# Kernel tuning notes

Measured on AMD Instinct MI355X. Metric: run time of the kernel, lower is better.

Reference implementation:

```python
import jax, jax.numpy as jnp
import numpy as np

H, D_IN, D_Q, D_V = 8, 16, 32, 32
N = M = 4096


def setup_inputs() -> dict:
    key = jax.random.key(0)
    ks = jax.random.split(key, 12)
    s_in = 1.0 / np.sqrt(D_IN)
    s_fc = 1.0 / np.sqrt(H * D_V)
    return {
        "x": jax.random.normal(ks[0], (N, D_IN), jnp.float32),
        "y": jax.random.normal(ks[1], (M, D_IN), jnp.float32),
        # per-head stacked weights: [H, D_IN, D_Q/ D_V]
        "Wq": jax.random.uniform(ks[2], (H, D_IN, D_Q), jnp.float32, -s_in, s_in),
        "bq": jax.random.uniform(ks[3], (H, D_Q), jnp.float32, -s_in, s_in),
        "Wk": jax.random.uniform(ks[4], (H, D_IN, D_Q), jnp.float32, -s_in, s_in),
        "bk": jax.random.uniform(ks[5], (H, D_Q), jnp.float32, -s_in, s_in),
        "Wv": jax.random.uniform(ks[6], (H, D_IN, D_V), jnp.float32, -s_in, s_in),
        "bv": jax.random.uniform(ks[7], (H, D_V), jnp.float32, -s_in, s_in),
        "Wo": jax.random.uniform(ks[8], (H * D_V, D_IN), jnp.float32, -s_fc, s_fc),
        "bo": jax.random.uniform(ks[9], (D_IN,), jnp.float32, -s_fc, s_fc),
    }


def reference(x, y, Wq, bq, Wk, bk, Wv, bv, Wo, bo):
    # batched per-head projections (fuses the 8 tiny Linears of the torch loop)
    q = jnp.einsum("nd,hdq->hnq", x, Wq) + bq[:, None, :]   # [H, N, D_Q]
    k = jnp.einsum("md,hdq->hmq", y, Wk) + bk[:, None, :]   # [H, M, D_Q]
    v = jnp.einsum("md,hdv->hmv", y, Wv) + bv[:, None, :]   # [H, M, D_V]
    scores = jnp.einsum("hnq,hmq->hnm", q, k) / jnp.sqrt(jnp.float32(D_Q))
    attn = jax.nn.softmax(scores, axis=-1)                  # [H, N, M]
    heads = jnp.einsum("hnm,hmv->hnv", attn, v)             # [H, N, D_V]
    # torch.cat(head_outputs, dim=-1): head h occupies columns [h*D_V:(h+1)*D_V]
    concat = jnp.transpose(heads, (1, 0, 2)).reshape(x.shape[0], H * D_V)
    return concat @ Wo + bo                                  # [N, D_IN]
```

## Files before the change

kernel.cpp:

```cpp
#include <hip/hip_runtime.h>
#include <hip/hip_bf16.h>

typedef __attribute__((ext_vector_type(8))) short bf16x8;
typedef __attribute__((ext_vector_type(4))) float f32x4;
typedef unsigned short u16;
typedef unsigned int u32;

#define NH 8
#define NN 4096
#define MM 4096

__device__ __forceinline__ u16 f2bf(float f) {
  u32 b = __float_as_uint(f);
  b += 0x7FFFu + ((b >> 16) & 1u);
  return (u16)(b >> 16);
}

__device__ __forceinline__ u32 pack_rnu(float a, float b) {
  u32 ua = __float_as_uint(a) + 0x8000u;
  u32 ub = __float_as_uint(b) + 0x8000u;
#if __has_builtin(__builtin_amdgcn_perm)
  return __builtin_amdgcn_perm(ub, ua, 0x07060302u);
#else
  return (ua >> 16) | (ub & 0xFFFF0000u);
#endif
}

#if __has_builtin(__builtin_amdgcn_exp2f)
__device__ __forceinline__ float exp2_fast(float x) { return __builtin_amdgcn_exp2f(x); }
#else
__device__ __forceinline__ float exp2_fast(float x) { return __expf(x * 0.69314718055994531f); }
#endif

__global__ __launch_bounds__(256) void proj_kernel(
    const float* __restrict__ x, const float* __restrict__ y,
    const float* __restrict__ Wq, const float* __restrict__ bq,
    const float* __restrict__ Wk, const float* __restrict__ bk,
    const float* __restrict__ Wv, const float* __restrict__ bv,
    u16* __restrict__ qs, u16* __restrict__ ks, u16* __restrict__ vT)
{
  __shared__ u16 sv[256][33];
  const int bid = blockIdx.x;
  const int tid = threadIdx.x;
  if (bid < 256) {
    int idx = bid * 256 + tid;
    int t = idx >> 15;
    int h = (idx >> 12) & 7;
    int row = idx & 4095;
    const float* src = (t ? y : x) + row * 16;
    const float* W = (t ? Wk : Wq) + (h << 9);
    const float* b = (t ? bk : bq) + (h << 5);
    const float scale = t ? 1.0f : 0.25503635116465163f;
    float4 r4[4];
#pragma unroll
    for (int i = 0; i < 4; ++i) r4[i] = ((const float4*)src)[i];
    const float* r = (const float*)r4;
    u16* out = (t ? ks : qs) + (idx & 32767) * 32;
#pragma unroll
    for (int j = 0; j < 32; ++j) {
      float a = b[j];
#pragma unroll
      for (int i = 0; i < 16; ++i) a = fmaf(r[i], W[i * 32 + j], a);
      out[j] = f2bf(a * scale);
    }
  } else {
    int vb = bid - 256;
    int h = vb >> 4;
    int kb = (vb & 15) << 8;
    const float* src = y + (kb + tid) * 16;
    const float* W = Wv + (h << 9);
    const float* b = bv + (h << 5);
    float4 r4[4];
#pragma unroll
    for (int i = 0; i < 4; ++i) r4[i] = ((const float4*)src)[i];
    const float* r = (const float*)r4;
#pragma unroll
    for (int j = 0; j < 32; ++j) {
      float a = b[j];
#pragma unroll
      for (int i = 0; i < 16; ++i) a = fmaf(r[i], W[i * 32 + j], a);
      sv[tid][j] = f2bf(a);
    }
    __syncthreads();
    int dv = tid >> 3;
    int c = (tid & 7) << 5;
    u16* dst = vT + (((h << 5) + dv) << 12) + kb + c;
#pragma unroll
    for (int q = 0; q < 4; ++q) {
      uint4 w;
      w.x = (u32)sv[c + 4 * q + 0][dv]      | ((u32)sv[c + 4 * q + 1][dv] << 16);
      w.y = (u32)sv[c + 4 * q + 2][dv]      | ((u32)sv[c + 4 * q + 3][dv] << 16);
      w.z = (u32)sv[c + 16 + 4 * q + 0][dv] | ((u32)sv[c + 16 + 4 * q + 1][dv] << 16);
      w.w = (u32)sv[c + 16 + 4 * q + 2][dv] | ((u32)sv[c + 16 + 4 * q + 3][dv] << 16);
      *(uint4*)(dst + q * 8) = w;
    }
  }
}

#define KST 40
#define VST 72
#define VSZ (32 * VST)

__global__ __launch_bounds__(256) void flash_kernel(
    const u16* __restrict__ qs, const u16* __restrict__ ksrc,
    const u16* __restrict__ vT, float* __restrict__ accP,
    float* __restrict__ lsumP)
{
  __shared__ u16 sK[128 * KST];
  __shared__ u16 sVT[2 * VSZ];
  const int h = blockIdx.y;
  const int qt = blockIdx.x;
  const int z = blockIdx.z;
  const int nIter = (MM / 128) / gridDim.z;
  const int kb0 = z * (MM / gridDim.z);
  const int tid = threadIdx.x;
  const int wv = tid >> 6;
  const int lane = tid & 63;
  const int d = lane & 15;
  const int g = lane >> 4;
  const int qrowA = (qt << 7) + (wv << 5) + d;
  const int qrowB = qrowA + 16;

  union U4 { uint4 q; bf16x8 v; };
  U4 qfA, qfB;
  qfA.q = *(const uint4*)(qs + (((h << 12) + qrowA) << 5) + (g << 3));
  qfB.q = *(const uint4*)(qs + (((h << 12) + qrowB) << 5) + (g << 3));

  union { u32 w[4]; bf16x8 v; } ones;
  {
    u32 ow = (d == 0) ? 0x3F803F80u : 0u;
    ones.w[0] = ow; ones.w[1] = ow; ones.w[2] = ow; ones.w[3] = ow;
  }

  f32x4 accA0 = {0.f, 0.f, 0.f, 0.f}, accA1 = {0.f, 0.f, 0.f, 0.f};
  f32x4 accB0 = {0.f, 0.f, 0.f, 0.f}, accB1 = {0.f, 0.f, 0.f, 0.f};
  f32x4 accLA = {0.f, 0.f, 0.f, 0.f}, accLB = {0.f, 0.f, 0.f, 0.f};
  const f32x4 zero = {0.f, 0.f, 0.f, 0.f};

  const u16* gK = ksrc + (h << 17) + (kb0 << 5) + ((tid >> 1) << 5) + ((tid & 1) << 4);
  const u16* gV = vT + (((h << 5) + (tid >> 3)) << 12) + kb0 + ((tid & 7) << 4);
  u16* wK = sK + (tid >> 1) * KST + ((tid & 1) << 4);
  u16* wV = sVT + ((tid & 7) >> 2) * VSZ + (tid >> 3) * VST + ((tid & 7) & 3) * 16;

  {
    uint4 a = *(const uint4*)gK, b = *(const uint4*)(gK + 8);
    uint4 c = *(const uint4*)gV, e = *(const uint4*)(gV + 8);
    *(uint4*)wK = a; *(uint4*)(wK + 8) = b;
    *(uint4*)wV = c; *(uint4*)(wV + 8) = e;
  }
  __syncthreads();

  auto compute = [&](const u16* kb, const u16* vb) {
    U4 kf[4];
#pragma unroll
    for (int t = 0; t < 4; ++t)
      kf[t].q = *(const uint4*)(kb + (t * 16 + d) * KST + (g << 3));

    union { u32 w[4]; bf16x8 v; } pbA0, pbA1, pbB0, pbB1;
    {
      f32x4 s0, s1, s2, s3;
      s0 = __builtin_amdgcn_mfma_f32_16x16x32_bf16(kf[0].v, qfA.v, zero, 0, 0, 0);
      s1 = __builtin_amdgcn_mfma_f32_16x16x32_bf16(kf[1].v, qfA.v, zero, 0, 0, 0);
      s2 = __builtin_amdgcn_mfma_f32_16x16x32_bf16(kf[2].v, qfA.v, zero, 0, 0, 0);
      s3 = __builtin_amdgcn_mfma_f32_16x16x32_bf16(kf[3].v, qfA.v, zero, 0, 0, 0);
      float e[16];
      e[0]=exp2_fast(s0.x); e[1]=exp2_fast(s0.y); e[2]=exp2_fast(s0.z); e[3]=exp2_fast(s0.w);
      e[4]=exp2_fast(s1.x); e[5]=exp2_fast(s1.y); e[6]=exp2_fast(s1.z); e[7]=exp2_fast(s1.w);
      e[8]=exp2_fast(s2.x); e[9]=exp2_fast(s2.y); e[10]=exp2_fast(s2.z); e[11]=exp2_fast(s2.w);
      e[12]=exp2_fast(s3.x); e[13]=exp2_fast(s3.y); e[14]=exp2_fast(s3.z); e[15]=exp2_fast(s3.w);
      pbA0.w[0] = pack_rnu(e[0], e[1]);   pbA0.w[1] = pack_rnu(e[2], e[3]);
      pbA0.w[2] = pack_rnu(e[4], e[5]);   pbA0.w[3] = pack_rnu(e[6], e[7]);
      pbA1.w[0] = pack_rnu(e[8], e[9]);   pbA1.w[1] = pack_rnu(e[10], e[11]);
      pbA1.w[2] = pack_rnu(e[12], e[13]); pbA1.w[3] = pack_rnu(e[14], e[15]);
    }
    {
      f32x4 s0, s1, s2, s3;
      s0 = __builtin_amdgcn_mfma_f32_16x16x32_bf16(kf[0].v, qfB.v, zero, 0, 0, 0);
      s1 = __builtin_amdgcn_mfma_f32_16x16x32_bf16(kf[1].v, qfB.v, zero, 0, 0, 0);
      s2 = __builtin_amdgcn_mfma_f32_16x16x32_bf16(kf[2].v, qfB.v, zero, 0, 0, 0);
      s3 = __builtin_amdgcn_mfma_f32_16x16x32_bf16(kf[3].v, qfB.v, zero, 0, 0, 0);
      float e[16];
      e[0]=exp2_fast(s0.x); e[1]=exp2_fast(s0.y); e[2]=exp2_fast(s0.z); e[3]=exp2_fast(s0.w);
      e[4]=exp2_fast(s1.x); e[5]=exp2_fast(s1.y); e[6]=exp2_fast(s1.z); e[7]=exp2_fast(s1.w);
      e[8]=exp2_fast(s2.x); e[9]=exp2_fast(s2.y); e[10]=exp2_fast(s2.z); e[11]=exp2_fast(s2.w);
      e[12]=exp2_fast(s3.x); e[13]=exp2_fast(s3.y); e[14]=exp2_fast(s3.z); e[15]=exp2_fast(s3.w);
      pbB0.w[0] = pack_rnu(e[0], e[1]);   pbB0.w[1] = pack_rnu(e[2], e[3]);
      pbB0.w[2] = pack_rnu(e[4], e[5]);   pbB0.w[3] = pack_rnu(e[6], e[7]);
      pbB1.w[0] = pack_rnu(e[8], e[9]);   pbB1.w[1] = pack_rnu(e[10], e[11]);
      pbB1.w[2] = pack_rnu(e[12], e[13]); pbB1.w[3] = pack_rnu(e[14], e[15]);
    }
    accLA = __builtin_amdgcn_mfma_f32_16x16x32_bf16(ones.v, pbA0.v, accLA, 0, 0, 0);
    accLA = __builtin_amdgcn_mfma_f32_16x16x32_bf16(ones.v, pbA1.v, accLA, 0, 0, 0);
    accLB = __builtin_amdgcn_mfma_f32_16x16x32_bf16(ones.v, pbB0.v, accLB, 0, 0, 0);
    accLB = __builtin_amdgcn_mfma_f32_16x16x32_bf16(ones.v, pbB1.v, accLB, 0, 0, 0);
    U4 vf0, vf1, vf2, vf3;
    const u16* vp = vb + d * VST;
    vf0.q = *(const uint4*)(vp + (g << 3));
    vf1.q = *(const uint4*)(vp + 32 + (g << 3));
    vp += 16 * VST;
    vf2.q = *(const uint4*)(vp + (g << 3));
    vf3.q = *(const uint4*)(vp + 32 + (g << 3));
    accA0 = __builtin_amdgcn_mfma_f32_16x16x32_bf16(vf0.v, pbA0.v, accA0, 0, 0, 0);
    accA0 = __builtin_amdgcn_mfma_f32_16x16x32_bf16(vf1.v, pbA1.v, accA0, 0, 0, 0);
    accA1 = __builtin_amdgcn_mfma_f32_16x16x32_bf16(vf2.v, pbA0.v, accA1, 0, 0, 0);
    accA1 = __builtin_amdgcn_mfma_f32_16x16x32_bf16(vf3.v, pbA1.v, accA1, 0, 0, 0);
    accB0 = __builtin_amdgcn_mfma_f32_16x16x32_bf16(vf0.v, pbB0.v, accB0, 0, 0, 0);
    accB0 = __builtin_amdgcn_mfma_f32_16x16x32_bf16(vf1.v, pbB1.v, accB0, 0, 0, 0);
    accB1 = __builtin_amdgcn_mfma_f32_16x16x32_bf16(vf2.v, pbB0.v, accB1, 0, 0, 0);
    accB1 = __builtin_amdgcn_mfma_f32_16x16x32_bf16(vf3.v, pbB1.v, accB1, 0, 0, 0);
  };

#pragma unroll 1
  for (int it = 0; it < nIter; ++it) {
    uint4 a, b, c, e;
    if (it < nIter - 1) {
      gK += 4096; gV += 128;
      a = *(const uint4*)gK; b = *(const uint4*)(gK + 8);
      c = *(const uint4*)gV; e = *(const uint4*)(gV + 8);
    }
    compute(sK, sVT);
    compute(sK + 64 * KST, sVT + VSZ);
    __syncthreads();
    if (it < nIter - 1) {
      *(uint4*)wK = a; *(uint4*)(wK + 8) = b;
      *(uint4*)wV = c; *(uint4*)(wV + 8) = e;
      __syncthreads();
    }
  }

  if (g == 0) {
    lsumP[((z * NH + h) << 12) + qrowA] = accLA.x;
    lsumP[((z * NH + h) << 12) + qrowB] = accLB.x;
  }
  float* cpA = accP + z * (NN * 256) + (qrowA << 8) + (h << 5) + (g << 2);
  *(float4*)cpA        = make_float4(accA0.x, accA0.y, accA0.z, accA0.w);
  *(float4*)(cpA + 16) = make_float4(accA1.x, accA1.y, accA1.z, accA1.w);
  float* cpB = accP + z * (NN * 256) + (qrowB << 8) + (h << 5) + (g << 2);
  *(float4*)cpB        = make_float4(accB0.x, accB0.y, accB0.z, accB0.w);
  *(float4*)(cpB + 16) = make_float4(accB1.x, accB1.y, accB1.z, accB1.w);
}

__global__ __launch_bounds__(256) void out_fused_kernel(
    const float* __restrict__ accP, const float* __restrict__ lsumP,
    const float* __restrict__ Wo, const float* __restrict__ bo,
    float* __restrict__ out, int S)
{
  __shared__ float cn[4][256];
  __shared__ float sQ[4][4][16];
  const int tid = threadIdx.x;
  const int n0 = blockIdx.x << 2;

  {
    const int r = tid >> 6, u = tid & 63;
    const int n = n0 + r;
    float4 o = make_float4(0.f, 0.f, 0.f, 0.f);
    for (int s = 0; s < S; ++s) {
      const float4 v = *(const float4*)(accP + (size_t)s * (NN * 256) + (n << 8) + (u << 2));
      o.x += v.x; o.y += v.y; o.z += v.z; o.w += v.w;
    }
    const int hh = u >> 3;
    float l = 0.f;
    for (int s = 0; s < S; ++s) l += lsumP[((s * NH + hh) << 12) + n];
    const float inv = 1.0f / l;
    *(float4*)&cn[r][u << 2] = make_float4(o.x * inv, o.y * inv, o.z * inv, o.w * inv);
  }
  __syncthreads();

  {
    const int r = tid >> 6, ks = (tid >> 4) & 3, c = tid & 15;
    const float* cr = &cn[r][ks << 6];
    const float* wp = Wo + (ks << 6) * 16 + c;
    float a = 0.f;
#pragma unroll
    for (int jj = 0; jj < 64; ++jj) {
      const int j2 = (jj + (ks << 4)) & 63;
      a = fmaf(cr[j2], wp[j2 * 16], a);
    }
    sQ[r][ks][c] = a;
  }
  __syncthreads();

  if (tid < 64) {
    const int r = tid >> 4, c = tid & 15;
    float v = bo[c] + ((sQ[r][0][c] + sQ[r][1][c]) + (sQ[r][2][c] + sQ[r][3][c]));
    out[((n0 + r) << 4) + c] = v;
  }
}

extern "C" void kernel_launch(void* const* d_in, const int* in_sizes, int n_in,
                              void* d_out, int out_size, void* d_ws, size_t ws_size,
                              hipStream_t stream) {
  const float* x  = (const float*)d_in[0];
  const float* y  = (const float*)d_in[1];
  const float* Wq = (const float*)d_in[2];
  const float* bq = (const float*)d_in[3];
  const float* Wk = (const float*)d_in[4];
  const float* bk = (const float*)d_in[5];
  const float* Wv = (const float*)d_in[6];
  const float* bv = (const float*)d_in[7];
  const float* Wo = (const float*)d_in[8];
  const float* bo = (const float*)d_in[9];
  float* out = (float*)d_out;

  u16* qs = (u16*)d_ws;
  u16* ks = qs + (NH * NN * 32);
  u16* vT = ks + (NH * MM * 32);
  float* accP = (float*)(vT + (NH * MM * 32));
  const int S = (ws_size >= (size_t)(6 + 16) * 1024 * 1024 + 512 * 1024) ? 4 : 1;
  float* lsumP = accP + (size_t)S * (NN * 256);

  hipLaunchKernelGGL(proj_kernel, dim3(384), dim3(256), 0, stream,
                     x, y, Wq, bq, Wk, bk, Wv, bv, qs, ks, vT);
  hipLaunchKernelGGL(flash_kernel, dim3(32, NH, S), dim3(256), 0, stream,
                     qs, ks, vT, accP, lsumP);
  hipLaunchKernelGGL(out_fused_kernel, dim3(1024), dim3(256), 0, stream,
                     accP, lsumP, Wo, bo, out, S);
}
```

Before: 62.45 us.

## Double query rows per warp and compute row sums with VALU adds

Each wave now handles 64 query rows instead of 32, so every K/V fragment read from LDS is reused across four query tiles, and the grid's query dimension is halved. The softmax denominator is now accumulated with scalar float adds and cross-lane shuffles instead of extra MFMAs against a ones vector. This cuts LDS traffic and MFMA count per score. The cost is more registers and fewer blocks (16x8xS), which may lower occupancy and parallelism on a 256-CU device.

New measurement: 64.97 us. 1.04x slower.

```diff
diff --git a/kernel.cpp b/kernel.cpp
--- a/kernel.cpp
+++ b/kernel.cpp
@@ -118,23 +118,26 @@
   const int lane = tid & 63;
   const int d = lane & 15;
   const int g = lane >> 4;
-  const int qrowA = (qt << 7) + (wv << 5) + d;
+  const int qrowA = (qt << 8) + (wv << 6) + d;
   const int qrowB = qrowA + 16;
+  const int qrowC = qrowA + 32;
+  const int qrowD = qrowA + 48;
 
   union U4 { uint4 q; bf16x8 v; };
-  U4 qfA, qfB;
-  qfA.q = *(const uint4*)(qs + (((h << 12) + qrowA) << 5) + (g << 3));
-  qfB.q = *(const uint4*)(qs + (((h << 12) + qrowB) << 5) + (g << 3));
-
-  union { u32 w[4]; bf16x8 v; } ones;
+  U4 qfA, qfB, qfC, qfD;
   {
-    u32 ow = (d == 0) ? 0x3F803F80u : 0u;
-    ones.w[0] = ow; ones.w[1] = ow; ones.w[2] = ow; ones.w[3] = ow;
-  }
-
+    const u16* qb = qs + (((h << 12) + qrowA) << 5) + (g << 3);
+    qfA.q = *(const uint4*)qb;
+    qfB.q = *(const uint4*)(qb + (16 << 5));
+    qfC.q = *(const uint4*)(qb + (32 << 5));
+    qfD.q = *(const uint4*)(qb + (48 << 5));
+  }
+
+  float lsA = 0.f, lsB = 0.f, lsC = 0.f, lsD = 0.f;
   f32x4 accA0 = {0.f, 0.f, 0.f, 0.f}, accA1 = {0.f, 0.f, 0.f, 0.f};
   f32x4 accB0 = {0.f, 0.f, 0.f, 0.f}, accB1 = {0.f, 0.f, 0.f, 0.f};
-  f32x4 accLA = {0.f, 0.f, 0.f, 0.f}, accLB = {0.f, 0.f, 0.f, 0.f};
+  f32x4 accC0 = {0.f, 0.f, 0.f, 0.f}, accC1 = {0.f, 0.f, 0.f, 0.f};
+  f32x4 accD0 = {0.f, 0.f, 0.f, 0.f}, accD1 = {0.f, 0.f, 0.f, 0.f};
   const f32x4 zero = {0.f, 0.f, 0.f, 0.f};
 
   const u16* gK = ksrc + (h << 17) + (kb0 << 5) + ((tid >> 1) << 5) + ((tid & 1) << 4);
@@ -151,63 +154,52 @@
   __syncthreads();
 
   auto compute = [&](const u16* kb, const u16* vb) {
-    U4 kf[4];
-#pragma unroll
-    for (int t = 0; t < 4; ++t)
-      kf[t].q = *(const uint4*)(kb + (t * 16 + d) * KST + (g << 3));
-
-    union { u32 w[4]; bf16x8 v; } pbA0, pbA1, pbB0, pbB1;
+    U4 kf0, kf1, kf2, kf3;
+    kf0.q = *(const uint4*)(kb + (0 * 16 + d) * KST + (g << 3));
+    kf1.q = *(const uint4*)(kb + (1 * 16 + d) * KST + (g << 3));
+    kf2.q = *(const uint4*)(kb + (2 * 16 + d) * KST + (g << 3));
+    kf3.q = *(const uint4*)(kb + (3 * 16 + d) * KST + (g << 3));
+    U4 vf0, vf1, vf2, vf3;
     {
-      f32x4 s0, s1, s2, s3;
-      s0 = __builtin_amdgcn_mfma_f32_16x16x32_bf16(kf[0].v, qfA.v, zero, 0, 0, 0);
-      s1 = __builtin_amdgcn_mfma_f32_16x16x32_bf16(kf[1].v, qfA.v, zero, 0, 0, 0);
-      s2 = __builtin_amdgcn_mfma_f32_16x16x32_bf16(kf[2].v, qfA.v, zero, 0, 0, 0);
-      s3 = __builtin_amdgcn_mfma_f32_16x16x32_bf16(kf[3].v, qfA.v, zero, 0, 0, 0);
-      float e[16];
-      e[0]=exp2_fast(s0.x); e[1]=exp2_fast(s0.y); e[2]=exp2_fast(s0.z); e[3]=exp2_fast(s0.w);
-      e[4]=exp2_fast(s1.x); e[5]=exp2_fast(s1.y); e[6]=exp2_fast(s1.z); e[7]=exp2_fast(s1.w);
-      e[8]=exp2_fast(s2.x); e[9]=exp2_fast(s2.y); e[10]=exp2_fast(s2.z); e[11]=exp2_fast(s2.w);
-      e[12]=exp2_fast(s3.x); e[13]=exp2_fast(s3.y); e[14]=exp2_fast(s3.z); e[15]=exp2_fast(s3.w);
-      pbA0.w[0] = pack_rnu(e[0], e[1]);   pbA0.w[1] = pack_rnu(e[2], e[3]);
-      pbA0.w[2] = pack_rnu(e[4], e[5]);   pbA0.w[3] = pack_rnu(e[6], e[7]);
-      pbA1.w[0] = pack_rnu(e[8], e[9]);   pbA1.w[1] = pack_rnu(e[10], e[11]);
-      pbA1.w[2] = pack_rnu(e[12], e[13]); pbA1.w[3] = pack_rnu(e[14], e[15]);
-    }
-    {
-      f32x4 s0, s1, s2, s3;
-      s0 = __builtin_amdgcn_mfma_f32_16x16x32_bf16(kf[0].v, qfB.v, zero, 0, 0, 0);
-      s1 = __builtin_amdgcn_mfma_f32_16x16x32_bf16(kf[1].v, qfB.v, zero, 0, 0, 0);
-      s2 = __builtin_amdgcn_mfma_f32_16x16x32_bf16(kf[2].v, qfB.v, zero, 0, 0, 0);
-      s3 = __builtin_amdgcn_mfma_f32_16x16x32_bf16(kf[3].v, qfB.v, zero, 0, 0, 0);
-      float e[16];
-      e[0]=exp2_fast(s0.x); e[1]=exp2_fast(s0.y); e[2]=exp2_fast(s0.z); e[3]=exp2_fast(s0.w);
-      e[4]=exp2_fast(s1.x); e[5]=exp2_fast(s1.y); e[6]=exp2_fast(s1.z); e[7]=exp2_fast(s1.w);
-      e[8]=exp2_fast(s2.x); e[9]=exp2_fast(s2.y); e[10]=exp2_fast(s2.z); e[11]=exp2_fast(s2.w);
-      e[12]=exp2_fast(s3.x); e[13]=exp2_fast(s3.y); e[14]=exp2_fast(s3.z); e[15]=exp2_fast(s3.w);
-      pbB0.w[0] = pack_rnu(e[0], e[1]);   pbB0.w[1] = pack_rnu(e[2], e[3]);
-      pbB0.w[2] = pack_rnu(e[4], e[5]);   pbB0.w[3] = pack_rnu(e[6], e[7]);
-      pbB1.w[0] = pack_rnu(e[8], e[9]);   pbB1.w[1] = pack_rnu(e[10], e[11]);
-      pbB1.w[2] = pack_rnu(e[12], e[13]); pbB1.w[3] = pack_rnu(e[14], e[15]);
-    }
-    accLA = __builtin_amdgcn_mfma_f32_16x16x32_bf16(ones.v, pbA0.v, accLA, 0, 0, 0);
-    accLA = __builtin_amdgcn_mfma_f32_16x16x32_bf16(ones.v, pbA1.v, accLA, 0, 0, 0);
-    accLB = __builtin_amdgcn_mfma_f32_16x16x32_bf16(ones.v, pbB0.v, accLB, 0, 0, 0);
-    accLB = __builtin_amdgcn_mfma_f32_16x16x32_bf16(ones.v, pbB1.v, accLB, 0, 0, 0);
-    U4 vf0, vf1, vf2, vf3;
-    const u16* vp = vb + d * VST;
-    vf0.q = *(const uint4*)(vp + (g << 3));
-    vf1.q = *(const uint4*)(vp + 32 + (g << 3));
-    vp += 16 * VST;
-    vf2.q = *(const uint4*)(vp + (g << 3));
-    vf3.q = *(const uint4*)(vp + 32 + (g << 3));
-    accA0 = __builtin_amdgcn_mfma_f32_16x16x32_bf16(vf0.v, pbA0.v, accA0, 0, 0, 0);
-    accA0 = __builtin_amdgcn_mfma_f32_16x16x32_bf16(vf1.v, pbA1.v, accA0, 0, 0, 0);
-    accA1 = __builtin_amdgcn_mfma_f32_16x16x32_bf16(vf2.v, pbA0.v, accA1, 0, 0, 0);
-    accA1 = __builtin_amdgcn_mfma_f32_16x16x32_bf16(vf3.v, pbA1.v, accA1, 0, 0, 0);
-    accB0 = __builtin_amdgcn_mfma_f32_16x16x32_bf16(vf0.v, pbB0.v, accB0, 0, 0, 0);
-    accB0 = __builtin_amdgcn_mfma_f32_16x16x32_bf16(vf1.v, pbB1.v, accB0, 0, 0, 0);
-    accB1 = __builtin_amdgcn_mfma_f32_16x16x32_bf16(vf2.v, pbB0.v, accB1, 0, 0, 0);
-    accB1 = __builtin_amdgcn_mfma_f32_16x16x32_bf16(vf3.v, pbB1.v, accB1, 0, 0, 0);
+      const u16* vp = vb + d * VST;
+      vf0.q = *(const uint4*)(vp + (g << 3));
+      vf1.q = *(const uint4*)(vp + 32 + (g << 3));
+      vp += 16 * VST;
+      vf2.q = *(const uint4*)(vp + (g << 3));
+      vf3.q = *(const uint4*)(vp + 32 + (g << 3));
+    }
+#define QTILE(QF, ACC0, ACC1, LS)                                              \
+    {                                                                          \
+      f32x4 s0, s1, s2, s3;                                                    \
+      s0 = __builtin_amdgcn_mfma_f32_16x16x32_bf16(kf0.v, QF.v, zero, 0, 0, 0);\
+      s1 = __builtin_amdgcn_mfma_f32_16x16x32_bf16(kf1.v, QF.v, zero, 0, 0, 0);\
+      s2 = __builtin_amdgcn_mfma_f32_16x16x32_bf16(kf2.v, QF.v, zero, 0, 0, 0);\
+      s3 = __builtin_amdgcn_mfma_f32_16x16x32_bf16(kf3.v, QF.v, zero, 0, 0, 0);\
+      float e0 = exp2_fast(s0.x), e1 = exp2_fast(s0.y);                        \
+      float e2 = exp2_fast(s0.z), e3 = exp2_fast(s0.w);                        \
+      float e4 = exp2_fast(s1.x), e5 = exp2_fast(s1.y);                        \
+      float e6 = exp2_fast(s1.z), e7 = exp2_fast(s1.w);                        \
+      float e8 = exp2_fast(s2.x), e9 = exp2_fast(s2.y);                        \
+      float e10 = exp2_fast(s2.z), e11 = exp2_fast(s2.w);                      \
+      float e12 = exp2_fast(s3.x), e13 = exp2_fast(s3.y);                      \
+      float e14 = exp2_fast(s3.z), e15 = exp2_fast(s3.w);                      \
+      LS += (((e0 + e1) + (e2 + e3)) + ((e4 + e5) + (e6 + e7)))                \
+          + (((e8 + e9) + (e10 + e11)) + ((e12 + e13) + (e14 + e15)));         \
+      union { u32 w[4]; bf16x8 v; } pb0, pb1;                                  \
+      pb0.w[0] = pack_rnu(e0, e1);   pb0.w[1] = pack_rnu(e2, e3);              \
+      pb0.w[2] = pack_rnu(e4, e5);   pb0.w[3] = pack_rnu(e6, e7);              \
+      pb1.w[0] = pack_rnu(e8, e9);   pb1.w[1] = pack_rnu(e10, e11);            \
+      pb1.w[2] = pack_rnu(e12, e13); pb1.w[3] = pack_rnu(e14, e15);            \
+      ACC0 = __builtin_amdgcn_mfma_f32_16x16x32_bf16(vf0.v, pb0.v, ACC0, 0, 0, 0); \
+      ACC0 = __builtin_amdgcn_mfma_f32_16x16x32_bf16(vf1.v, pb1.v, ACC0, 0, 0, 0); \
+      ACC1 = __builtin_amdgcn_mfma_f32_16x16x32_bf16(vf2.v, pb0.v, ACC1, 0, 0, 0); \
+      ACC1 = __builtin_amdgcn_mfma_f32_16x16x32_bf16(vf3.v, pb1.v, ACC1, 0, 0, 0); \
+    }
+    QTILE(qfA, accA0, accA1, lsA)
+    QTILE(qfB, accB0, accB1, lsB)
+    QTILE(qfC, accC0, accC1, lsC)
+    QTILE(qfD, accD0, accD1, lsD)
+#undef QTILE
   };
 
 #pragma unroll 1
@@ -228,16 +220,27 @@
     }
   }
 
+  lsA += __shfl_xor(lsA, 16);  lsA += __shfl_xor(lsA, 32);
+  lsB += __shfl_xor(lsB, 16);  lsB += __shfl_xor(lsB, 32);
+  lsC += __shfl_xor(lsC, 16);  lsC += __shfl_xor(lsC, 32);
+  lsD += __shfl_xor(lsD, 16);  lsD += __shfl_xor(lsD, 32);
   if (g == 0) {
-    lsumP[((z * NH + h) << 12) + qrowA] = accLA.x;
-    lsumP[((z * NH + h) << 12) + qrowB] = accLB.x;
-  }
-  float* cpA = accP + z * (NN * 256) + (qrowA << 8) + (h << 5) + (g << 2);
-  *(float4*)cpA        = make_float4(accA0.x, accA0.y, accA0.z, accA0.w);
-  *(float4*)(cpA + 16) = make_float4(accA1.x, accA1.y, accA1.z, accA1.w);
-  float* cpB = accP + z * (NN * 256) + (qrowB << 8) + (h << 5) + (g << 2);
-  *(float4*)cpB        = make_float4(accB0.x, accB0.y, accB0.z, accB0.w);
-  *(float4*)(cpB + 16) = make_float4(accB1.x, accB1.y, accB1.z, accB1.w);
+    lsumP[((z * NH + h) << 12) + qrowA] = lsA;
+    lsumP[((z * NH + h) << 12) + qrowB] = lsB;
+    lsumP[((z * NH + h) << 12) + qrowC] = lsC;
+    lsumP[((z * NH + h) << 12) + qrowD] = lsD;
+  }
+#define STORE_ACC(QROW, A0, A1)                                                \
+  {                                                                            \
+    float* cp = accP + z * (NN * 256) + ((QROW) << 8) + (h << 5) + (g << 2);   \
+    *(float4*)cp        = make_float4(A0.x, A0.y, A0.z, A0.w);                 \
+    *(float4*)(cp + 16) = make_float4(A1.x, A1.y, A1.z, A1.w);                 \
+  }
+  STORE_ACC(qrowA, accA0, accA1)
+  STORE_ACC(qrowB, accB0, accB1)
+  STORE_ACC(qrowC, accC0, accC1)
+  STORE_ACC(qrowD, accD0, accD1)
+#undef STORE_ACC
 }
 
 __global__ __launch_bounds__(256) void out_fused_kernel(
@@ -311,7 +314,7 @@
 
   hipLaunchKernelGGL(proj_kernel, dim3(384), dim3(256), 0, stream,
                      x, y, Wq, bq, Wk, bk, Wv, bv, qs, ks, vT);
-  hipLaunchKernelGGL(flash_kernel, dim3(32, NH, S), dim3(256), 0, stream,
+  hipLaunchKernelGGL(flash_kernel, dim3(16, NH, S), dim3(256), 0, stream,
                      qs, ks, vT, accP, lsumP);
   hipLaunchKernelGGL(out_fused_kernel, dim3(1024), dim3(256), 0, stream,
                      accP, lsumP, Wo, bo, out, S);
```
